# Kernel tuning notes

Hardware: AMD Instinct MI355X
Metric: run time of the kernel (lower is better)

Reference implementation:

```python
import jax, jax.numpy as jnp
import numpy as np

B, C, N, T = 8, 32, 4000, 12
KT = 3
TS = 6          # tem_size
SUP_ORD_CH = (2 * 3 + 1) * C  # (order*support_len+1)*c_in = 224
EPS = 1e-5


def setup_inputs() -> dict:
    key = jax.random.key(0)
    ks = jax.random.split(key, 20)
    inp = {
        "x": jax.random.normal(ks[0], (B, C, N, T), dtype=jnp.float32),
        # dense normalized supports (scaled uniform, like row-normalized adjacency)
        "A0": jax.random.uniform(ks[1], (N, N), dtype=jnp.float32) / N,
        "A1": jax.random.uniform(ks[2], (N, N), dtype=jnp.float32) / N,
        "A2": jax.random.uniform(ks[3], (N, N), dtype=jnp.float32) / N,
        # conv1: 1x1 Conv2d(32 -> 32), bias
        "conv1_w": jax.random.normal(ks[4], (C, C), dtype=jnp.float32) * 0.05,
        "conv1_b": jnp.zeros((C,), dtype=jnp.float32),
        # multigcn mlp: Conv2d(224 -> 64, kernel (1, Kt)), bias
        "mlp_w": jax.random.normal(ks[5], (2 * C, SUP_ORD_CH, 1, KT), dtype=jnp.float32) * 0.02,
        "mlp_b": jnp.zeros((2 * C,), dtype=jnp.float32),
        # conv_temp1: 1x1 Conv2d over time axis (10 -> 6), bias
        "ct1_w": jax.random.normal(ks[6], (TS, T - KT + 1), dtype=jnp.float32) * 0.1,
        "ct1_b": jnp.zeros((TS,), dtype=jnp.float32),
        # TATT_1 params
        "tat_c1_w": jax.random.normal(ks[7], (C,), dtype=jnp.float32) * 0.1,   # Conv2d(c_in->1,1x1,no bias)
        "tat_c2_w": jax.random.normal(ks[8], (N,), dtype=jnp.float32) * 0.01,  # Conv2d(N->1,1x1,no bias)
        "tat_w": jax.random.normal(ks[9], (N, C), dtype=jnp.float32) * 0.01,
        "tat_bias": jnp.zeros((TS, TS), dtype=jnp.float32),
        "tat_v": jax.random.normal(ks[10], (TS, TS), dtype=jnp.float32) * 0.3,
        "bn1_g": jnp.ones((TS,), dtype=jnp.float32),
        "bn1_b": jnp.zeros((TS,), dtype=jnp.float32),
        # final BatchNorm2d(c_out)
        "bn2_g": jnp.ones((C,), dtype=jnp.float32),
        "bn2_b": jnp.zeros((C,), dtype=jnp.float32),
    }
    return inp


def reference(x, A0, A1, A2, conv1_w, conv1_b, mlp_w, mlp_b, ct1_w, ct1_b,
              tat_c1_w, tat_c2_w, tat_w, tat_bias, tat_v, bn1_g, bn1_b,
              bn2_g, bn2_b):
    # residual = conv1(x)  (1x1 conv over channels)
    residual = jnp.einsum('oc,bcnl->bonl', conv1_w, x) + conv1_b[None, :, None, None]

    # multi_gcn_time: nconv does A<-A.T then einsum('ncvl,vw->ncwl'),
    # i.e. out[..,w,..] = sum_v x[..,v,..] * A[w,v]
    outs = [x]
    for A in (A0, A1, A2):
        x1 = jnp.einsum('bcvl,wv->bcwl', x, A)
        outs.append(x1)
        x2 = jnp.einsum('bcvl,wv->bcwl', x1, A)
        outs.append(x2)
    h = jnp.concatenate(outs, axis=1)  # (B, 224, N, T)
    h = jax.lax.conv_general_dilated(
        h, mlp_w, window_strides=(1, 1), padding='VALID',
        dimension_numbers=('NCHW', 'OIHW', 'NCHW')) + mlp_b[None, :, None, None]  # (B,64,N,10)

    # gated tanh * sigmoid
    x1, x2 = jnp.split(h, 2, axis=1)
    g = jnp.tanh(x1) * jax.nn.sigmoid(x2)  # (B,32,N,10)

    # conv_temp1: 1x1 conv over the TIME axis (10 -> 6)
    g = jnp.einsum('ql,bcnl->bcnq', ct1_w, g) + ct1_b[None, None, None, :]  # (B,32,N,6)

    # TATT_1 temporal attention coefficients
    f1 = jnp.einsum('c,bcnt->btn', tat_c1_w, g)                       # (B,6,N)
    f2 = jnp.einsum('n,bcnt->bct', tat_c2_w, g)                       # (B,32,6)
    logits = jax.nn.sigmoid(jnp.einsum('btn,nc,bcs->bts', f1, tat_w, f2) + tat_bias)
    logits = jnp.einsum('ts,bsq->btq', tat_v, logits)                 # (B,6,6)
    # BatchNorm1d(tem_size) applied after permute(0,2,1): channel = q axis
    lp = jnp.transpose(logits, (0, 2, 1))
    mu = lp.mean(axis=(0, 2), keepdims=True)
    var = lp.var(axis=(0, 2), keepdims=True)
    lp = (lp - mu) / jnp.sqrt(var + EPS) * bn1_g[None, :, None] + bn1_b[None, :, None]
    logits = jnp.transpose(lp, (0, 2, 1))
    coefs = jax.nn.softmax(logits, axis=-1)                           # (B,6,6)

    # x = einsum('bcnl,blq->bcnq', x, T_coef.transpose(-1,-2))
    Tc = jnp.transpose(coefs, (0, 2, 1))
    out = jnp.einsum('bcnl,blq->bcnq', g, Tc)                         # (B,32,N,6)

    y = out + residual[:, :, :, -out.shape[3]:]
    # BatchNorm2d(c_out), training-mode batch stats
    mu2 = y.mean(axis=(0, 2, 3), keepdims=True)
    var2 = y.var(axis=(0, 2, 3), keepdims=True)
    return (y - mu2) / jnp.sqrt(var2 + EPS) * bn2_g[None, :, None, None] + bn2_b[None, :, None, None]
```

## Files before the change

kernel.cpp:

```cpp
#include <hip/hip_runtime.h>
#include <hip/hip_bf16.h>
#include <cstdint>
#include <cstddef>


typedef __attribute__((ext_vector_type(8))) short s16x8;
typedef __attribute__((ext_vector_type(4))) short s16x4;
typedef __attribute__((ext_vector_type(4))) float f32x4;

#define DEVFN __device__ __forceinline__

DEVFN void gload16(const void* g, void* l) {
  __builtin_amdgcn_global_load_lds((const __attribute__((address_space(1))) unsigned int*)g,
                                   (__attribute__((address_space(3))) unsigned int*)l, 16, 0, 0);
}

DEVFN unsigned short f2bf(float f) {
  union { float f; unsigned int u; } v; v.f = f;
  unsigned int u = v.u;
  return (unsigned short)((u + 0x7fffu + ((u >> 16) & 1u)) >> 16);
}

__global__ void k_transpose(const float* __restrict__ x,
                            unsigned short* __restrict__ Xt,
                            unsigned short* __restrict__ Scat) {
  __shared__ float ldsT[32 * 417];
  int v0 = blockIdx.x * 32;
  int b = blockIdx.y;
  int tid = threadIdx.x;
  for (int i = tid; i < 1024; i += 256) {
    int c = i >> 5, vv = i & 31;
    const float* src = x + ((size_t)(b * 32 + c) * 4000 + v0 + vv) * 12;
    f32x4 a0 = *(const f32x4*)(src);
    f32x4 a1 = *(const f32x4*)(src + 4);
    f32x4 a2 = *(const f32x4*)(src + 8);
    float* d = ldsT + c * 417 + vv * 13;
    d[0] = a0.x; d[1] = a0.y; d[2] = a0.z; d[3] = a0.w;
    d[4] = a1.x; d[5] = a1.y; d[6] = a1.z; d[7] = a1.w;
    d[8] = a2.x; d[9] = a2.y; d[10] = a2.z; d[11] = a2.w;
  }
  __syncthreads();
  for (int unit = tid; unit < 384; unit += 256) {
    int l = unit >> 5, c = unit & 31;
    alignas(16) unsigned short tmp[32];
#pragma unroll
    for (int vv = 0; vv < 32; ++vv) tmp[vv] = f2bf(ldsT[c * 417 + vv * 13 + l]);
    unsigned short* dst = Xt + (size_t)(b * 384 + l * 32 + c) * 4096 + v0;
#pragma unroll
    for (int j = 0; j < 4; ++j) *(s16x8*)(dst + j * 8) = *(const s16x8*)(tmp + j * 8);
  }
  for (int unit = tid; unit < 384; unit += 256) {
    int l = unit >> 5, vv = unit & 31;
    alignas(16) unsigned short tmp[32];
#pragma unroll
    for (int c = 0; c < 32; ++c) tmp[c] = f2bf(ldsT[c * 417 + vv * 13 + l]);
    int bn = b * 4000 + v0 + vv;
    unsigned short* dst = Scat + ((((size_t)l * 500 + (bn >> 6)) * 28) * 64 + (bn & 63)) * 8;
#pragma unroll
    for (int j = 0; j < 4; ++j) *(s16x8*)(dst + j * 512) = *(const s16x8*)(tmp + j * 8);
  }
}

__global__ void k_castA(const float* __restrict__ A, unsigned short* __restrict__ Abf) {
  int idx = blockIdx.x * 256 + threadIdx.x;
  int r = idx >> 10;
  int c4 = (idx & 1023) << 2;
  alignas(8) unsigned short o[4] = {0, 0, 0, 0};
  if (r < 4000 && c4 < 4000) {
    f32x4 v = *(const f32x4*)(A + (size_t)r * 4000 + c4);
    o[0] = f2bf(v.x); o[1] = f2bf(v.y); o[2] = f2bf(v.z); o[3] = f2bf(v.w);
  }
  *(s16x4*)(Abf + (size_t)r * 4096 + c4) = *(const s16x4*)o;
}

__global__ void k_wcat(const float* __restrict__ mlp_w, unsigned short* __restrict__ Wcat) {
  int i = blockIdx.x * 256 + threadIdx.x;
  if (i >= 43008) return;
  int e = i & 7;
  int j = (i >> 3) % 21;
  int rs = (i >> 3) / 21;
  int s = rs & 1, row = rs >> 1;
  int kt = j / 7, ks = j % 7;
  int p2 = row >> 6, g = (row >> 4) & 3, lr = row & 15;
  int oc = (s ? 32 : 0) + p2 * 16 + lr;
  int ic = ks * 32 + g * 8 + e;
  Wcat[i] = f2bf(mlp_w[((size_t)oc * 224 + ic) * 3 + kt]);
}

#define MFMA_(a, b, c) __builtin_amdgcn_mfma_f32_16x16x32_bf16(a, b, c, 0, 0, 0)

#define STGA(d, t) do {                                                          \
    const unsigned short* _s = aSrc + (size_t)(t) * 64;                          \
    unsigned short* _l = smem + (d) * 12288;                                     \
    gload16(_s,          _l + tid * 8);                                          \
    gload16(_s + 262144, _l + (512 + tid) * 8);                                  \
    gload16(_s + 524288, _l + (1024 + tid) * 8);                                 \
  } while (0)

#define STGB(d, h, t) do {                                                       \
    const unsigned short* _s = bSrc + (size_t)(h) * 524288 + (size_t)(t) * 64;   \
    unsigned short* _l = smem + 24576 + ((d) * 2 + (h)) * 8192;                  \
    gload16(_s,          _l + tid * 8);                                          \
    gload16(_s + 262144, _l + (512 + tid) * 8);                                  \
  } while (0)

#define LDA_(d, f, kk) (*(const s16x8*)(smem + (d) * 12288 + aoff + (f) * 1024 + ((kk) ? sxor : 0)))
#define LDB_(d, nf, kk) (*(const s16x8*)(smem + 24576 + ((d) * 2 + hb) * 8192 + boff + (nf) * 1024 + ((kk) ? sxor : 0)))

#define PHASE(d, mp, FIRST, STAGE_CODE, VM) do {                                 \
    s16x8 a00 = LDA_(d, 2 * (mp), 0),     a01 = LDA_(d, 2 * (mp), 1);            \
    s16x8 a10 = LDA_(d, 2 * (mp) + 1, 0), a11 = LDA_(d, 2 * (mp) + 1, 1);        \
    if (FIRST) {                                                                 \
      _Pragma("unroll")                                                          \
      for (int nf = 0; nf < 4; ++nf) { bfr[nf][0] = LDB_(d, nf, 0); bfr[nf][1] = LDB_(d, nf, 1); } \
    }                                                                            \
    STAGE_CODE;                                                                  \
    if (VM) asm volatile("s_waitcnt vmcnt(2)" ::: "memory");                     \
    __builtin_amdgcn_s_barrier();                                                \
    asm volatile("s_waitcnt lgkmcnt(0)" ::: "memory");                           \
    __builtin_amdgcn_s_setprio(1);                                               \
    _Pragma("unroll")                                                            \
    for (int nf = 0; nf < 4; ++nf) {                                             \
      acc[2 * (mp)][nf]     = MFMA_(a00, bfr[nf][0], acc[2 * (mp)][nf]);         \
      acc[2 * (mp)][nf]     = MFMA_(a01, bfr[nf][1], acc[2 * (mp)][nf]);         \
      acc[2 * (mp) + 1][nf] = MFMA_(a10, bfr[nf][0], acc[2 * (mp) + 1][nf]);     \
      acc[2 * (mp) + 1][nf] = MFMA_(a11, bfr[nf][1], acc[2 * (mp) + 1][nf]);     \
    }                                                                            \
    __builtin_amdgcn_s_setprio(0);                                               \
  } while (0)

template <int WRITE_C1>
__global__ __launch_bounds__(512, 2)
void k_gemm(const unsigned short* __restrict__ P, const unsigned short* __restrict__ Q,
            unsigned short* __restrict__ C1, unsigned short* __restrict__ Scat, int jslot) {
  extern __shared__ unsigned short smem[];
  int tid = threadIdx.x;
  int w = tid >> 6, lane = tid & 63;
  int lr = lane & 15, g = lane >> 4;
  int mq = w >> 2, nq = w & 3;
  int bid = blockIdx.x;
  int xcd = bid & 7, lid = bid >> 3;
  int nt = xcd * 2 + (lid >> 4);
  int mt = lid & 15;
  int m0 = mt * 192, n0 = nt * 256;
  int hb = nq >> 1;
  int slot0 = (g ^ (lr & 7)) * 8;
  int sxor = (slot0 & 32) ? -32 : 32;
  int aoff = (mq * 96 + lr) * 64 + slot0;
  int boff = ((nq & 1) * 64 + lr) * 64 + slot0;
  int gk = ((tid & 7) ^ ((tid >> 3) & 7)) * 8;
  const unsigned short* aSrc = P + (size_t)(m0 + (tid >> 3)) * 4096 + gk;
  const unsigned short* bSrc = Q + (size_t)(n0 + (tid >> 3)) * 4096 + gk;
  f32x4 acc[6][4] = {};
  s16x8 bfr[4][2];

  STGA(0, 0);
  STGB(0, 0, 0); STGB(0, 1, 0);
  STGB(1, 0, 1);
  asm volatile("s_waitcnt vmcnt(2)" ::: "memory");
  __builtin_amdgcn_s_barrier();

#pragma unroll 1
  for (int i = 0; i < 32; ++i) {
    int t1 = 2 * i + 1, t2 = 2 * i + 2, t3 = 2 * i + 3;
    PHASE(0, 0, 1, STGB(1, 1, t1), 0);
    PHASE(0, 1, 0, STGA(1, t1),    0);
    PHASE(0, 2, 0, STGB(0, 0, t2), 1);
    PHASE(1, 0, 1, STGB(0, 1, t2), 0);
    PHASE(1, 1, 0, STGA(0, t2),    0);
    PHASE(1, 2, 0, STGB(1, 0, t3), 1);
  }

  asm volatile("s_waitcnt vmcnt(0) lgkmcnt(0)" ::: "memory");
  __syncthreads();
  unsigned short* eld = smem;
  int rb = g * 4;
#pragma unroll
  for (int f = 0; f < 6; ++f)
#pragma unroll
    for (int nf = 0; nf < 4; ++nf)
#pragma unroll
      for (int r = 0; r < 4; ++r)
        eld[(mq * 96 + f * 16 + rb + r) * 264 + nq * 64 + nf * 16 + lr] = f2bf(acc[f][nf][r]);
  __syncthreads();
  if (WRITE_C1) {
#pragma unroll
    for (int uu = 0; uu < 2; ++uu) {
      int u = uu * 512 + tid;
      if (u < 768) {
        int row = u >> 2, q = u & 3;
        unsigned short* dst = C1 + (size_t)(m0 + row) * 4096 + n0 + q * 64;
        const unsigned short* sp = eld + row * 264 + q * 64;
#pragma unroll
        for (int j = 0; j < 8; ++j) *(s16x8*)(dst + j * 8) = *(const s16x8*)(sp + j * 8);
      }
    }
  }
  int bb2 = m0 / 384, lb = (m0 % 384) >> 5;
#pragma unroll
  for (int uu = 0; uu < 3; ++uu) {
    int u = uu * 512 + tid;
    int lg = u >> 8, nl = u & 255;
    int node = n0 + nl;
    if (node < 4000) {
      alignas(16) unsigned short tmp[32];
#pragma unroll
      for (int c = 0; c < 32; ++c) tmp[c] = eld[(lg * 32 + c) * 264 + nl];
      int bn = bb2 * 4000 + node;
      int l2 = lb + lg;
      unsigned short* d2 = Scat + ((((size_t)l2 * 500 + (bn >> 6)) * 28 + jslot) * 64 + (bn & 63)) * 8;
#pragma unroll
      for (int j = 0; j < 4; ++j) *(s16x8*)(d2 + j * 512) = *(const s16x8*)(tmp + j * 8);
    }
  }
}

#define MLPSTG(L, BUF) do {                                                    \
    const unsigned short* _sb = Scat + ((size_t)(L) * 500 + grp) * 14336;      \
    unsigned short* _lb = lds + (BUF) * 14336;                                 \
    gload16(_sb + tid * 8,          _lb + tid * 8);                            \
    gload16(_sb + (512 + tid) * 8,  _lb + (512 + tid) * 8);                    \
    gload16(_sb + (1024 + tid) * 8, _lb + (1024 + tid) * 8);                   \
    if (tid < 256) gload16(_sb + (1536 + tid) * 8, _lb + (1536 + tid) * 8);    \
  } while (0)

__global__ __launch_bounds__(512, 2)
void k_mlp(const unsigned short* __restrict__ Wcat, const unsigned short* __restrict__ Scat,
           const float* __restrict__ mlp_b, const float* __restrict__ ct1_w,
           const float* __restrict__ ct1_b, float* __restrict__ g6) {
  __shared__ unsigned short lds[2 * 14336];
  int tid = threadIdx.x;
  int grp = blockIdx.x;
  int w = tid >> 6, lane = tid & 63;
  int lr = lane & 15, g = lane >> 4;
  int p2 = w & 1, bnq = w >> 1;
  const unsigned short* wrow = Wcat + (size_t)(((p2 * 4 + g) * 16 + lr) * 2) * 168;
  s16x8 wa[21], wb[21];
#pragma unroll
  for (int j = 0; j < 21; ++j) {
    wa[j] = *(const s16x8*)(wrow + j * 8);
    wb[j] = *(const s16x8*)(wrow + 168 + j * 8);
  }
  float mb1[4], mb2[4];
#pragma unroll
  for (int r = 0; r < 4; ++r) {
    mb1[r] = mlp_b[p2 * 16 + g * 4 + r];
    mb2[r] = mlp_b[32 + p2 * 16 + g * 4 + r];
  }
  f32x4 acc[3][2];
  float g6a[4][6] = {};

  MLPSTG(0, 0);
  asm volatile("s_waitcnt vmcnt(0)" ::: "memory");
  __syncthreads();

#pragma unroll
  for (int l = 0; l < 12; ++l) {
    if (l < 11) MLPSTG(l + 1, (l + 1) & 1);
    if (l <= 9) {
      acc[l % 3][0] = (f32x4){0.f, 0.f, 0.f, 0.f};
      acc[l % 3][1] = (f32x4){0.f, 0.f, 0.f, 0.f};
    }
    const unsigned short* sb = lds + (l & 1) * 14336;
#pragma unroll
    for (int kt = 0; kt < 3; ++kt) {
      int t = l - kt;
      if (t < 0 || t > 9) continue;
      int st = t % 3;
#pragma unroll
      for (int ks = 0; ks < 7; ++ks) {
        int j = kt * 7 + ks;
        s16x8 bb = *(const s16x8*)(sb + ((ks * 4 + g) * 64 + bnq * 16 + lr) * 8);
        acc[st][0] = MFMA_(wa[j], bb, acc[st][0]);
        acc[st][1] = MFMA_(wb[j], bb, acc[st][1]);
      }
    }
    if (l >= 2) {
      int t = l - 2, st = t % 3;
#pragma unroll
      for (int r = 0; r < 4; ++r) {
        float v1 = acc[st][0][r] + mb1[r];
        float v2 = acc[st][1][r] + mb2[r];
        float gg = tanhf(v1) * (1.0f / (1.0f + __expf(-v2)));
#pragma unroll
        for (int q6 = 0; q6 < 6; ++q6) g6a[r][q6] += ct1_w[q6 * 10 + t] * gg;
      }
    }
    asm volatile("s_waitcnt vmcnt(0)" ::: "memory");
    __syncthreads();
  }

  int nglob = grp * 64 + bnq * 16 + lr;
  int b = nglob / 4000, nn = nglob - b * 4000;
#pragma unroll
  for (int r = 0; r < 4; ++r) {
    int c = p2 * 16 + g * 4 + r;
    float* op = g6 + ((size_t)(b * 32 + c) * 4000 + nn) * 6;
#pragma unroll
    for (int q6 = 0; q6 < 6; ++q6) op[q6] = g6a[r][q6] + ct1_b[q6];
  }
}

__global__ void k_f1(const float* __restrict__ g6, const float* __restrict__ c1,
                     float* __restrict__ f1) {
  int idx = blockIdx.x * 128 + threadIdx.x;
  if (idx >= 8 * 4000) return;
  int n = idx % 4000, b = idx / 4000;
  float acc[6] = {};
  const float* gp = g6 + ((size_t)b * 32 * 4000 + n) * 6;
  for (int c = 0; c < 32; ++c) {
    float wv = c1[c];
    const float* p = gp + (size_t)c * 4000 * 6;
#pragma unroll
    for (int t = 0; t < 6; ++t) acc[t] += wv * p[t];
  }
  for (int t = 0; t < 6; ++t) f1[((size_t)b * 6 + t) * 4000 + n] = acc[t];
}

__global__ void k_f2(const float* __restrict__ g6, const float* __restrict__ c2,
                     float* __restrict__ f2) {
  __shared__ float red[256 * 6];
  int bc = blockIdx.x;
  int tid = threadIdx.x;
  float acc[6] = {};
  const float* gp = g6 + (size_t)bc * 4000 * 6;
  for (int n = tid; n < 4000; n += 256) {
    float wv = c2[n];
#pragma unroll
    for (int t = 0; t < 6; ++t) acc[t] += wv * gp[(size_t)n * 6 + t];
  }
  for (int t = 0; t < 6; ++t) red[tid * 6 + t] = acc[t];
  __syncthreads();
  for (int s = 128; s > 0; s >>= 1) {
    if (tid < s)
      for (int t = 0; t < 6; ++t) red[tid * 6 + t] += red[(tid + s) * 6 + t];
    __syncthreads();
  }
  if (tid < 6) f2[bc * 6 + tid] = red[tid];
}

__global__ void k_m1(const float* __restrict__ f1, const float* __restrict__ tw,
                     float* __restrict__ m1) {
  __shared__ float red[8][32];
  int bt = blockIdx.x;
  int nc = blockIdx.y;
  int tid = threadIdx.x;
  int c = tid & 31, gi = tid >> 5;
  float acc = 0.f;
  const float* fp = f1 + (size_t)bt * 4000 + nc * 250;
  const float* twp = tw + ((size_t)nc * 250) * 32 + c;
  for (int n = gi; n < 250; n += 8) acc += fp[n] * twp[n * 32];
  red[gi][c] = acc;
  __syncthreads();
  if (tid < 32) {
    float s = 0.f;
#pragma unroll
    for (int gg = 0; gg < 8; ++gg) s += red[gg][c];
    atomicAdd(&m1[(size_t)bt * 32 + c], s);
  }
}

__global__ void k_att(const float* __restrict__ m1, const float* __restrict__ f2,
                      const float* __restrict__ bias, const float* __restrict__ tv,
                      const float* __restrict__ g1, const float* __restrict__ b1,
                      float* __restrict__ coefs) {
  __shared__ float sig[48 * 6], lgs[48 * 6], mu[6], iv[6];
  int tid = threadIdx.x;
  int b = tid / 6, t = tid % 6;
  if (tid < 48) {
    for (int s = 0; s < 6; ++s) {
      float a = bias[t * 6 + s];
      for (int c = 0; c < 32; ++c)
        a += m1[((size_t)b * 6 + t) * 32 + c] * f2[((size_t)b * 32 + c) * 6 + s];
      sig[tid * 6 + s] = 1.0f / (1.0f + __expf(-a));
    }
  }
  __syncthreads();
  if (tid < 48) {
    for (int q = 0; q < 6; ++q) {
      float a = 0.f;
      for (int s = 0; s < 6; ++s) a += tv[t * 6 + s] * sig[(b * 6 + s) * 6 + q];
      lgs[tid * 6 + q] = a;
    }
  }
  __syncthreads();
  if (tid < 6) {
    float s = 0, s2 = 0;
    for (int r = 0; r < 48; ++r) { float v = lgs[r * 6 + tid]; s += v; s2 += v * v; }
    float m = s / 48.f;
    mu[tid] = m;
    iv[tid] = rsqrtf(s2 / 48.f - m * m + 1e-5f);
  }
  __syncthreads();
  if (tid < 48) {
    float v[6], mx = -1e30f;
    for (int q = 0; q < 6; ++q) {
      v[q] = (lgs[tid * 6 + q] - mu[q]) * iv[q] * g1[q] + b1[q];
      mx = fmaxf(mx, v[q]);
    }
    float s = 0;
    for (int q = 0; q < 6; ++q) { v[q] = __expf(v[q] - mx); s += v[q]; }
    float inv = 1.0f / s;
    for (int q = 0; q < 6; ++q) coefs[tid * 6 + q] = v[q] * inv;
  }
}

__global__ void k_final1(const float* __restrict__ x, const float* __restrict__ cw,
                         const float* __restrict__ cb, const float* __restrict__ g6,
                         const float* __restrict__ coefs, float* __restrict__ out) {
  __shared__ float xt[32 * 8 * 6];
  __shared__ float cwT[1024];
  __shared__ float cfs[36], cbs[32];
  int n0 = blockIdx.x * 8;
  int b = blockIdx.y;
  int tid = threadIdx.x;
  {
    int ci = tid >> 3, seg = tid & 7;
    const float* xp = x + ((size_t)(b * 32 + ci) * 4000 + n0 + seg) * 12 + 6;
#pragma unroll
    for (int q = 0; q < 6; ++q) xt[(ci * 8 + seg) * 6 + q] = xp[q];
  }
  for (int i = tid; i < 1024; i += 256) { int o = i >> 5, ci = i & 31; cwT[ci * 32 + o] = cw[i]; }
  if (tid < 36) cfs[tid] = coefs[b * 36 + tid];
  if (tid < 32) cbs[tid] = cb[tid];
  __syncthreads();
  int nn = tid & 7, c = tid >> 3;
  const float* gp = g6 + ((size_t)(b * 32 + c) * 4000 + n0 + nn) * 6;
  float gv[6];
#pragma unroll
  for (int l = 0; l < 6; ++l) gv[l] = gp[l];
  float y[6];
#pragma unroll
  for (int q = 0; q < 6; ++q) {
    float at = 0.f;
#pragma unroll
    for (int l = 0; l < 6; ++l) at += gv[l] * cfs[q * 6 + l];
    y[q] = at + cbs[c];
  }
  for (int ci = 0; ci < 32; ++ci) {
    float wv = cwT[ci * 32 + c];
#pragma unroll
    for (int q = 0; q < 6; ++q) y[q] += wv * xt[(ci * 8 + nn) * 6 + q];
  }
  float* op = out + ((size_t)(b * 32 + c) * 4000 + n0 + nn) * 6;
#pragma unroll
  for (int q = 0; q < 6; ++q) op[q] = y[q];
}

__global__ void k_stats(const float* __restrict__ out, float* __restrict__ stats) {
  __shared__ float r1[4], r2[4];
  int bc = blockIdx.y;
  int c = bc & 31;
  int tid = threadIdx.x;
  const float* p = out + (size_t)bc * 24000 + blockIdx.x * 6000;
  float s = 0.f, s2 = 0.f;
  for (int i = tid * 4; i < 6000; i += 1024) {
    f32x4 v = *(const f32x4*)(p + i);
    s  += v.x + v.y + v.z + v.w;
    s2 += v.x * v.x + v.y * v.y + v.z * v.z + v.w * v.w;
  }
#pragma unroll
  for (int off = 32; off > 0; off >>= 1) {
    s  += __shfl_down(s, off);
    s2 += __shfl_down(s2, off);
  }
  int lane = tid & 63, w = tid >> 6;
  if (lane == 0) { r1[w] = s; r2[w] = s2; }
  __syncthreads();
  if (tid == 0) {
    atomicAdd(&stats[c],      r1[0] + r1[1] + r1[2] + r1[3]);
    atomicAdd(&stats[32 + c], r2[0] + r2[1] + r2[2] + r2[3]);
  }
}

__global__ void k_final2(float* __restrict__ out, const float* __restrict__ stats,
                         const float* __restrict__ g2, const float* __restrict__ b2) {
  int idx = (blockIdx.x * 256 + threadIdx.x) * 4;
  if (idx >= 6144000) return;
  int c = (idx / 24000) % 32;
  float mean = stats[c] * (1.0f / 192000.f);
  float var = stats[32 + c] * (1.0f / 192000.f) - mean * mean;
  float sc = rsqrtf(var + 1e-5f) * g2[c];
  float sh = b2[c] - mean * sc;
  f32x4 v = *(f32x4*)(out + idx);
  v.x = v.x * sc + sh; v.y = v.y * sc + sh; v.z = v.z * sc + sh; v.w = v.w * sc + sh;
  *(f32x4*)(out + idx) = v;
}

extern "C" void kernel_launch(void* const* d_in, const int* in_sizes, int n_in,
                              void* d_out, int out_size, void* d_ws, size_t ws_size,
                              hipStream_t stream) {
  (void)in_sizes; (void)n_in; (void)out_size;
  const float* x       = (const float*)d_in[0];
  const float* A[3]    = {(const float*)d_in[1], (const float*)d_in[2], (const float*)d_in[3]};
  const float* conv1_w = (const float*)d_in[4];
  const float* conv1_b = (const float*)d_in[5];
  const float* mlp_w   = (const float*)d_in[6];
  const float* mlp_b   = (const float*)d_in[7];
  const float* ct1_w   = (const float*)d_in[8];
  const float* ct1_b   = (const float*)d_in[9];
  const float* c1w     = (const float*)d_in[10];
  const float* c2w     = (const float*)d_in[11];
  const float* tw      = (const float*)d_in[12];
  const float* tbias   = (const float*)d_in[13];
  const float* tv      = (const float*)d_in[14];
  const float* bn1g    = (const float*)d_in[15];
  const float* bn1b    = (const float*)d_in[16];
  const float* bn2g    = (const float*)d_in[17];
  const float* bn2b    = (const float*)d_in[18];
  float* out = (float*)d_out;

  char* ws = (char*)d_ws;
  size_t off = 0;
  auto alloc = [&](size_t bytes) { size_t r = off; off += (bytes + 255) & ~(size_t)255; return r; };
  size_t oScat = alloc(172032000);
  size_t oXt   = alloc(25165824);
  size_t oA    = alloc(33554432);
  size_t oY1t  = alloc(25165824);
  size_t oWcat = alloc(86016);
  size_t oF1 = alloc(768000);
  size_t oF2 = alloc(6144);
  size_t oM1 = alloc(6144);
  size_t oCf = alloc(1152);
  size_t oSt = alloc(256);
  if (ws_size < off) return;

  unsigned short* Scat = (unsigned short*)(ws + oScat);
  unsigned short* Xt   = (unsigned short*)(ws + oXt);
  float*          g6   = (float*)(ws + oXt);
  unsigned short* Abf  = (unsigned short*)(ws + oA);
  unsigned short* Y1t  = (unsigned short*)(ws + oY1t);
  unsigned short* Wcat = (unsigned short*)(ws + oWcat);

  hipFuncSetAttribute((const void*)k_gemm<0>, hipFuncAttributeMaxDynamicSharedMemorySize, 114688);
  hipFuncSetAttribute((const void*)k_gemm<1>, hipFuncAttributeMaxDynamicSharedMemorySize, 114688);

  hipMemsetAsync(Xt, 0, 25165824, stream);
  hipMemsetAsync(ws + oSt, 0, 256, stream);
  hipMemsetAsync(ws + oM1, 0, 6144, stream);
  k_transpose<<<dim3(125, 8), 256, 0, stream>>>(x, Xt, Scat);
  k_wcat<<<168, 256, 0, stream>>>(mlp_w, Wcat);
  for (int i = 0; i < 3; ++i) {
    k_castA<<<16384, 256, 0, stream>>>(A[i], Abf);
    k_gemm<1><<<256, 512, 114688, stream>>>(Xt, Abf, Y1t, Scat, (2 * i + 1) * 4);
    k_gemm<0><<<256, 512, 114688, stream>>>(Y1t, Abf, nullptr, Scat, (2 * i + 2) * 4);
  }
  k_mlp<<<500, 512, 0, stream>>>(Wcat, Scat, mlp_b, ct1_w, ct1_b, g6);
  k_f1<<<250, 128, 0, stream>>>(g6, c1w, (float*)(ws + oF1));
  k_f2<<<256, 256, 0, stream>>>(g6, c2w, (float*)(ws + oF2));
  k_m1<<<dim3(48, 16), 256, 0, stream>>>((float*)(ws + oF1), tw, (float*)(ws + oM1));
  k_att<<<1, 64, 0, stream>>>((float*)(ws + oM1), (float*)(ws + oF2), tbias, tv, bn1g, bn1b,
                              (float*)(ws + oCf));
  k_final1<<<dim3(500, 8), 256, 0, stream>>>(x, conv1_w, conv1_b, g6, (float*)(ws + oCf), out);
  k_stats<<<dim3(4, 256), 256, 0, stream>>>(out, (float*)(ws + oSt));
  k_final2<<<6000, 256, 0, stream>>>(out, (float*)(ws + oSt), bn2g, bn2b);
}
```

Before: 761.2 us.

## Triple-buffer A tiles in GEMM pipeline to prefetch two k-steps ahead

The GEMM main loop now keeps three LDS buffers for the A operand instead of two and issues A loads two k-tiles ahead, with rotating buffer indices and adjusted vmcnt waits. The aim is to hide more global-load latency behind the MFMA work. In exchange, LDS use per block rises to 136 KB and the loop carries extra index arithmetic and guard conditions on the tail iterations. With __launch_bounds__(512,2), two blocks would need about 272 KB of LDS, which likely exceeds the per-CU capacity and drops occupancy to one block per CU.

```diff
diff --git a/kernel.cpp b/kernel.cpp
--- a/kernel.cpp
+++ b/kernel.cpp
@@ -89,33 +89,34 @@
 
 #define MFMA_(a, b, c) __builtin_amdgcn_mfma_f32_16x16x32_bf16(a, b, c, 0, 0, 0)
 
-#define STGA(d, t) do {                                                          \
+#define STGA3(ab, t) do {                                                        \
     const unsigned short* _s = aSrc + (size_t)(t) * 64;                          \
-    unsigned short* _l = smem + (d) * 12288;                                     \
+    unsigned short* _l = smem + (ab) * 12288;                                    \
     gload16(_s,          _l + tid * 8);                                          \
     gload16(_s + 262144, _l + (512 + tid) * 8);                                  \
     gload16(_s + 524288, _l + (1024 + tid) * 8);                                 \
   } while (0)
 
-#define STGB(d, h, t) do {                                                       \
+#define STGB3(pr, h, t) do {                                                     \
     const unsigned short* _s = bSrc + (size_t)(h) * 524288 + (size_t)(t) * 64;   \
-    unsigned short* _l = smem + 24576 + ((d) * 2 + (h)) * 8192;                  \
+    unsigned short* _l = smem + 36864 + ((pr) * 2 + (h)) * 8192;                 \
     gload16(_s,          _l + tid * 8);                                          \
     gload16(_s + 262144, _l + (512 + tid) * 8);                                  \
   } while (0)
 
-#define LDA_(d, f, kk) (*(const s16x8*)(smem + (d) * 12288 + aoff + (f) * 1024 + ((kk) ? sxor : 0)))
-#define LDB_(d, nf, kk) (*(const s16x8*)(smem + 24576 + ((d) * 2 + hb) * 8192 + boff + (nf) * 1024 + ((kk) ? sxor : 0)))
-
-#define PHASE(d, mp, FIRST, STAGE_CODE, VM) do {                                 \
-    s16x8 a00 = LDA_(d, 2 * (mp), 0),     a01 = LDA_(d, 2 * (mp), 1);            \
-    s16x8 a10 = LDA_(d, 2 * (mp) + 1, 0), a11 = LDA_(d, 2 * (mp) + 1, 1);        \
+#define LDA3(ab, f, kk) (*(const s16x8*)(smem + (ab) * 12288 + aoff + (f) * 1024 + ((kk) ? sxor : 0)))
+#define LDB3(pr, nf, kk) (*(const s16x8*)(smem + 36864 + ((pr) * 2 + hb) * 8192 + boff + (nf) * 1024 + ((kk) ? sxor : 0)))
+
+#define PHASE3(ab, pr, mp, FIRST, STAGE_CODE, VM) do {                           \
+    s16x8 a00 = LDA3(ab, 2 * (mp), 0),     a01 = LDA3(ab, 2 * (mp), 1);          \
+    s16x8 a10 = LDA3(ab, 2 * (mp) + 1, 0), a11 = LDA3(ab, 2 * (mp) + 1, 1);      \
     if (FIRST) {                                                                 \
       _Pragma("unroll")                                                          \
-      for (int nf = 0; nf < 4; ++nf) { bfr[nf][0] = LDB_(d, nf, 0); bfr[nf][1] = LDB_(d, nf, 1); } \
+      for (int nf = 0; nf < 4; ++nf) { bfr[nf][0] = LDB3(pr, nf, 0); bfr[nf][1] = LDB3(pr, nf, 1); } \
     }                                                                            \
     STAGE_CODE;                                                                  \
-    if (VM) asm volatile("s_waitcnt vmcnt(2)" ::: "memory");                     \
+    if ((VM) == 1)      asm volatile("s_waitcnt vmcnt(5)" ::: "memory");         \
+    else if ((VM) == 2) asm volatile("s_waitcnt vmcnt(0)" ::: "memory");         \
     __builtin_amdgcn_s_barrier();                                                \
     asm volatile("s_waitcnt lgkmcnt(0)" ::: "memory");                           \
     __builtin_amdgcn_s_setprio(1);                                               \
@@ -154,21 +155,23 @@
   f32x4 acc[6][4] = {};
   s16x8 bfr[4][2];
 
-  STGA(0, 0);
-  STGB(0, 0, 0); STGB(0, 1, 0);
-  STGB(1, 0, 1);
-  asm volatile("s_waitcnt vmcnt(2)" ::: "memory");
+  STGA3(0, 0);
+  STGB3(0, 0, 0);
+  STGB3(0, 1, 0);
+  STGA3(1, 1);
+  STGB3(1, 0, 1);
+  asm volatile("s_waitcnt vmcnt(5)" ::: "memory");
   __builtin_amdgcn_s_barrier();
 
+  int a0 = 0;
 #pragma unroll 1
-  for (int i = 0; i < 32; ++i) {
-    int t1 = 2 * i + 1, t2 = 2 * i + 2, t3 = 2 * i + 3;
-    PHASE(0, 0, 1, STGB(1, 1, t1), 0);
-    PHASE(0, 1, 0, STGA(1, t1),    0);
-    PHASE(0, 2, 0, STGB(0, 0, t2), 1);
-    PHASE(1, 0, 1, STGB(0, 1, t2), 0);
-    PHASE(1, 1, 0, STGA(0, t2),    0);
-    PHASE(1, 2, 0, STGB(1, 0, t3), 1);
+  for (int t = 0; t < 64; ++t) {
+    int bt = t & 1;
+    int a2 = a0 + 2; if (a2 >= 3) a2 -= 3;
+    PHASE3(a0, bt, 0, 1, if (t <= 62) STGB3(bt ^ 1, 1, t + 1), 0);
+    PHASE3(a0, bt, 1, 0, if (t <= 61) STGA3(a2, t + 2),        0);
+    PHASE3(a0, bt, 2, 0, if (t <= 61) STGB3(bt, 0, t + 2),     (t >= 62) ? 2 : 1);
+    a0 = (a0 == 2) ? 0 : a0 + 1;
   }
 
   asm volatile("s_waitcnt vmcnt(0) lgkmcnt(0)" ::: "memory");
@@ -532,8 +535,8 @@
   unsigned short* Y1t  = (unsigned short*)(ws + oY1t);
   unsigned short* Wcat = (unsigned short*)(ws + oWcat);
 
-  hipFuncSetAttribute((const void*)k_gemm<0>, hipFuncAttributeMaxDynamicSharedMemorySize, 114688);
-  hipFuncSetAttribute((const void*)k_gemm<1>, hipFuncAttributeMaxDynamicSharedMemorySize, 114688);
+  hipFuncSetAttribute((const void*)k_gemm<0>, hipFuncAttributeMaxDynamicSharedMemorySize, 139264);
+  hipFuncSetAttribute((const void*)k_gemm<1>, hipFuncAttributeMaxDynamicSharedMemorySize, 139264);
 
   hipMemsetAsync(Xt, 0, 25165824, stream);
   hipMemsetAsync(ws + oSt, 0, 256, stream);
@@ -542,8 +545,8 @@
   k_wcat<<<168, 256, 0, stream>>>(mlp_w, Wcat);
   for (int i = 0; i < 3; ++i) {
     k_castA<<<16384, 256, 0, stream>>>(A[i], Abf);
-    k_gemm<1><<<256, 512, 114688, stream>>>(Xt, Abf, Y1t, Scat, (2 * i + 1) * 4);
-    k_gemm<0><<<256, 512, 114688, stream>>>(Y1t, Abf, nullptr, Scat, (2 * i + 2) * 4);
+    k_gemm<1><<<256, 512, 139264, stream>>>(Xt, Abf, Y1t, Scat, (2 * i + 1) * 4);
+    k_gemm<0><<<256, 512, 139264, stream>>>(Y1t, Abf, nullptr, Scat, (2 * i + 2) * 4);
   }
   k_mlp<<<500, 512, 0, stream>>>(Wcat, Scat, mlp_b, ct1_w, ct1_b, g6);
   k_f1<<<250, 128, 0, stream>>>(g6, c1w, (float*)(ws + oF1));
```

Result: no change. 774.5 us (+1.8%).
